# Kernel tuning notes

Hardware: AMD Instinct MI355X
Metric: run time of the kernel (lower is better)

## Reference

```python
import jax, jax.numpy as jnp
import numpy as np

MIN_C = 1e-6
MIN_NORM = 1e-15
BALL_EPS = 0.004  # float32 ball epsilon


def _norm(x):
    return jnp.maximum(jnp.linalg.norm(x, axis=-1, keepdims=True), MIN_NORM)


def _project(x, c):
    norm = _norm(x)
    maxnorm = (1.0 - BALL_EPS) / jnp.sqrt(c)
    return jnp.where(norm > maxnorm, x / norm * maxnorm, x)


def _tanh(x):
    return jnp.tanh(jnp.clip(x, -15.0, 15.0))


def _artanh(x):
    x = jnp.clip(x, -1.0 + 1e-5, 1.0 - 1e-5)
    return 0.5 * (jnp.log1p(x) - jnp.log1p(-x))


def _expmap0(u, c):
    sc = jnp.sqrt(c)
    n = _norm(u)
    return _project(_tanh(sc * n) * u / (sc * n), c)


def _logmap0(y, c):
    sc = jnp.sqrt(c)
    n = _norm(y)
    return y / n / sc * _artanh(sc * n)


def _mobius_add(x, y, c):
    x2 = jnp.sum(x * x, -1, keepdims=True)
    y2 = jnp.sum(y * y, -1, keepdims=True)
    xy = jnp.sum(x * y, -1, keepdims=True)
    num = (1 + 2 * c * xy + c * y2) * x + (1 - c * x2) * y
    den = jnp.maximum(1 + 2 * c * xy + c * c * x2 * y2, MIN_NORM)
    return num / den


N_NODE, N_EDGE, D, ATTN, B, N_VOCAB = 100000, 1000000, 64, 64, 256, 401


def setup_inputs() -> dict:
    key = jax.random.key(0)
    ks = jax.random.split(key, 12)
    r_idx = jax.random.randint(ks[0], (N_EDGE,), 0, B, dtype=jnp.int32)
    rel = jax.random.randint(ks[1], (N_EDGE,), 0, N_VOCAB, dtype=jnp.int32)
    sub = jax.random.randint(ks[2], (N_EDGE,), 0, N_NODE, dtype=jnp.int32)
    obj = jax.random.randint(ks[3], (N_EDGE,), 0, N_NODE, dtype=jnp.int32)
    zero = jnp.zeros((N_EDGE,), jnp.int32)
    edges = jnp.stack([r_idx, zero, rel, zero, sub, obj], axis=1)  # [E, 6]
    s = 0.1
    return {
        "hidden": jax.random.normal(ks[4], (N_NODE, D), jnp.float32) * s,
        "q_rel": jax.random.randint(ks[5], (B,), 0, N_VOCAB, dtype=jnp.int32),
        "edges": edges,
        "rela_embed": jax.random.normal(ks[6], (N_VOCAB, D), jnp.float32) * s,
        "Ws_w": jax.random.normal(ks[7], (ATTN, D), jnp.float32) * s,
        "Wr_w": jax.random.normal(ks[8], (ATTN, D), jnp.float32) * s,
        "Wqr_w": jax.random.normal(ks[9], (ATTN, D), jnp.float32) * s,
        "Wqr_b": jnp.zeros((ATTN,), jnp.float32),
        "Wattn_w": jax.random.normal(ks[10], (1, ATTN), jnp.float32) * s,
        "Wh_w": jax.random.normal(ks[11], (D, D), jnp.float32) * s,
        "n_node": N_NODE,
    }


def reference(hidden, q_rel, edges, rela_embed, Ws_w, Wr_w, Wqr_w, Wqr_b, Wattn_w, Wh_w, n_node):
    c = MIN_C
    sub, rel, obj, r_idx = edges[:, 4], edges[:, 2], edges[:, 5], edges[:, 0]
    hs = hidden[sub]                 # [E, D] gather
    hr = rela_embed[rel]             # [E, D]
    h_qr = rela_embed[q_rel][r_idx]  # [E, D]
    # attention MLP -> scalar gate per edge
    pre = hs @ Ws_w.T + hr @ Wr_w.T + h_qr @ Wqr_w.T + Wqr_b
    alpha = jax.nn.sigmoid(jax.nn.relu(pre) @ Wattn_w.T)  # [E, 1]
    # hyperbolic message
    hs_h = _expmap0(hs, c)
    hr_h = _expmap0(hr, c)
    mess2 = _logmap0(_project(_mobius_add(hs_h, hr_h, c), c), c)
    message = mess2 * alpha
    agg = jax.ops.segment_sum(message, obj, num_segments=n_node)  # scatter-add
    a = _expmap0(agg @ Wh_w.T, c)
    a = jax.nn.relu(a)  # act
    return _logmap0(a, c)
```

## Files before the change

kernel.cpp:

```cpp
#include <hip/hip_runtime.h>
#include <math.h>
#include <stdint.h>

#define N_NODE 100000
#define N_EDGE 1000000
#define DIM    64
#define NB     256
#define NVOCAB 401
#define SCAN_B 1024
#define NCHUNK ((N_NODE + SCAN_B - 1) / SCAN_B)
#define AGG_WAVES 8192
#define NSHARD 8
#define EPB 2048

typedef short short8  __attribute__((ext_vector_type(8)));
typedef float floatx4 __attribute__((ext_vector_type(4)));
typedef unsigned short ushort_t;

__device__ inline unsigned short f2bf_rne(float f)
{
    unsigned u = __float_as_uint(f);
    unsigned r = u + 0x7FFF + ((u >> 16) & 1);
    return (unsigned short)(r >> 16);
}
__device__ inline float bflo(unsigned u) { return __uint_as_float(u << 16); }
__device__ inline float bfhi(unsigned u) { return __uint_as_float(u & 0xFFFF0000u); }
__device__ inline unsigned short f2h(float f)
{
    _Float16 h = (_Float16)f;
    unsigned short s; __builtin_memcpy(&s, &h, 2); return s;
}
__device__ inline float h2f(unsigned b)
{
    unsigned short s = (unsigned short)b;
    _Float16 h; __builtin_memcpy(&h, &s, 2); return (float)h;
}

__device__ inline void split8(float4 v0, float4 v1, short8& hi, short8& lo)
{
    float f[8] = {v0.x, v0.y, v0.z, v0.w, v1.x, v1.y, v1.z, v1.w};
    #pragma unroll
    for (int j = 0; j < 8; ++j) {
        unsigned u = __float_as_uint(f[j]);
        unsigned r = u + 0x7FFF + ((u >> 16) & 1);
        unsigned short h = (unsigned short)(r >> 16);
        float hf = __uint_as_float(((unsigned)h) << 16);
        float l  = f[j] - hf;
        unsigned u2 = __float_as_uint(l);
        unsigned r2 = u2 + 0x7FFF + ((u2 >> 16) & 1);
        hi[j] = (short)h;
        lo[j] = (short)(r2 >> 16);
    }
}

__device__ void gemm64_body(
    const float* __restrict__ X,
    const int*   __restrict__ idx,
    const float* __restrict__ W,
    const float* __restrict__ bias,
    void* __restrict__ Yv,
    ushort_t* __restrict__ Y2,
    int R, int out_mode, int blk)
{
    int wave = threadIdx.x >> 6;
    int lane = threadIdx.x & 63;
    int m    = lane & 15;
    int quad = lane >> 4;
    int r0   = blk * 64 + wave * 16;

    int r = r0 + m;
    int src = (r < R) ? (idx ? idx[r] : r) : 0;
    const float* xrow = X + (size_t)src * DIM + quad * 8;

    float4 a0[2], a1[2];
    #pragma unroll
    for (int c = 0; c < 2; ++c) {
        a0[c] = *(const float4*)(xrow + 32 * c);
        a1[c] = *(const float4*)(xrow + 32 * c + 4);
    }
    short8 ah[2], al[2];
    #pragma unroll
    for (int c = 0; c < 2; ++c) split8(a0[c], a1[c], ah[c], al[c]);

    if (out_mode == 3 && r < R) {
        #pragma unroll
        for (int c = 0; c < 2; ++c)
            *(short8*)(Y2 + (size_t)r * DIM + 32 * c + quad * 8) = ah[c];
    }

    floatx4 acc[4] = {{0,0,0,0},{0,0,0,0},{0,0,0,0},{0,0,0,0}};
    #pragma unroll
    for (int g = 0; g < 4; ++g) {
        const float* wrow = W + (size_t)(g * 16 + m) * DIM + quad * 8;
        #pragma unroll
        for (int c = 0; c < 2; ++c) {
            float4 b0 = *(const float4*)(wrow + 32 * c);
            float4 b1 = *(const float4*)(wrow + 32 * c + 4);
            short8 bh, bl;
            split8(b0, b1, bh, bl);
            acc[g] = __builtin_amdgcn_mfma_f32_16x16x32_bf16(ah[c], bh, acc[g], 0, 0, 0);
            acc[g] = __builtin_amdgcn_mfma_f32_16x16x32_bf16(ah[c], bl, acc[g], 0, 0, 0);
            acc[g] = __builtin_amdgcn_mfma_f32_16x16x32_bf16(al[c], bh, acc[g], 0, 0, 0);
        }
    }

    #pragma unroll
    for (int g = 0; g < 4; ++g) {
        float bv = bias ? bias[g * 16 + m] : 0.0f;
        #pragma unroll
        for (int reg = 0; reg < 4; ++reg) {
            int rr = r0 + quad * 4 + reg;
            if (rr < R) {
                float v = acc[g][reg] + bv;
                if (out_mode == 1) v = fmaxf(v, 0.0f);
                if (out_mode >= 2)
                    ((ushort_t*)Yv)[(size_t)rr * DIM + g * 16 + m] = f2bf_rne(v);
                else
                    ((float*)Yv)[(size_t)rr * DIM + g * 16 + m] = v;
            }
        }
    }
}

__global__ __launch_bounds__(256) void gemm64_kernel(
    const float* __restrict__ X, const int* __restrict__ idx,
    const float* __restrict__ W, const float* __restrict__ bias,
    void* __restrict__ Yv, ushort_t* __restrict__ Y2, int R, int out_mode)
{
    gemm64_body(X, idx, W, bias, Yv, Y2, R, out_mode, blockIdx.x);
}

__global__ __launch_bounds__(256) void gemm64_bf16A_kernel(
    const ushort_t* __restrict__ A,
    const float* __restrict__ W,
    float* __restrict__ Y, int R)
{
    int wave = threadIdx.x >> 6;
    int lane = threadIdx.x & 63;
    int m    = lane & 15;
    int quad = lane >> 4;
    int r0   = blockIdx.x * 64 + wave * 16;

    int r = r0 + m;
    int src = (r < R) ? r : 0;
    short8 a8[2];
    #pragma unroll
    for (int c = 0; c < 2; ++c)
        a8[c] = *(const short8*)(A + (size_t)src * DIM + 32 * c + quad * 8);

    floatx4 acc[4] = {{0,0,0,0},{0,0,0,0},{0,0,0,0},{0,0,0,0}};
    #pragma unroll
    for (int g = 0; g < 4; ++g) {
        const float* wrow = W + (size_t)(g * 16 + m) * DIM + quad * 8;
        #pragma unroll
        for (int c = 0; c < 2; ++c) {
            float4 b0 = *(const float4*)(wrow + 32 * c);
            float4 b1 = *(const float4*)(wrow + 32 * c + 4);
            short8 bh, bl;
            split8(b0, b1, bh, bl);
            acc[g] = __builtin_amdgcn_mfma_f32_16x16x32_bf16(a8[c], bh, acc[g], 0, 0, 0);
            acc[g] = __builtin_amdgcn_mfma_f32_16x16x32_bf16(a8[c], bl, acc[g], 0, 0, 0);
        }
    }

    #pragma unroll
    for (int g = 0; g < 4; ++g) {
        #pragma unroll
        for (int reg = 0; reg < 4; ++reg) {
            int rr = r0 + quad * 4 + reg;
            if (rr < R)
                Y[(size_t)rr * DIM + g * 16 + m] = fmaxf(acc[g][reg], 0.0f);
        }
    }
}

#define G1 ((N_NODE + 63) / 64)
#define G2 ((NVOCAB + 63) / 64)
#define G3 (NB / 64)
#define GSMALL (G2 + G3)
#define GD8 ((N_EDGE + EPB - 1) / EPB)
#define PREP_T (G1 + GD8)
#define PREP_GRID (GSMALL + PREP_T)

__global__ __launch_bounds__(256) void prep_kernel(
    const float* __restrict__ hidden,
    const float* __restrict__ rela,
    const int*   __restrict__ q_rel,
    const float* __restrict__ Ws,
    const float* __restrict__ Wr,
    const float* __restrict__ Wqr,
    const float* __restrict__ Wqr_b,
    ushort_t* __restrict__ hsWs,
    ushort_t* __restrict__ hidb,
    ushort_t* __restrict__ rel_preb,
    ushort_t* __restrict__ relab,
    ushort_t* __restrict__ qr_preb,
    const int* __restrict__ edges,
    int* __restrict__ deg8,
    int* __restrict__ rank,
    int2* __restrict__ epack)
{
    int b = blockIdx.x;
    if (b < G2) {
        gemm64_body(rela, nullptr, Wr, nullptr, rel_preb, relab, NVOCAB, 3, b);
    } else if (b < GSMALL) {
        gemm64_body(rela, q_rel, Wqr, Wqr_b, qr_preb, nullptr, NB, 2, b - G2);
    } else {
        int bp = b - GSMALL;
        int prior = (int)(((long)bp * GD8) / PREP_T);
        int nxt   = (int)(((long)(bp + 1) * GD8) / PREP_T);
        if (nxt > prior) {
            int base = prior * EPB + threadIdx.x;
            #pragma unroll
            for (int k = 0; k < 8; ++k) {
                int e = base + k * 256;
                if (e < N_EDGE) {
                    int2 ab = *(const int2*)(edges + (size_t)e * 6);
                    int2 cd = *(const int2*)(edges + (size_t)e * 6 + 2);
                    int2 ef = *(const int2*)(edges + (size_t)e * 6 + 4);
                    epack[e] = make_int2(ef.x | (cd.x << 17), ef.y | (ab.x << 17));
                    int s = (e >> 11) & (NSHARD - 1);
                    rank[e] = atomicAdd(&deg8[s * N_NODE + ef.y], 1);
                }
            }
        } else {
            gemm64_body(hidden, nullptr, Ws, nullptr, hsWs, hidb, N_NODE, 3, bp - prior);
        }
    }
}

__global__ __launch_bounds__(SCAN_B) void scan1_kernel(const int* __restrict__ deg8,
                                                       int* __restrict__ partial)
{
    __shared__ int s[SCAN_B];
    int g = blockIdx.x * SCAN_B + threadIdx.x;
    int tot = 0;
    if (g < N_NODE)
        #pragma unroll
        for (int k = 0; k < NSHARD; ++k) tot += deg8[k * N_NODE + g];
    s[threadIdx.x] = tot;
    __syncthreads();
    for (int off = SCAN_B / 2; off; off >>= 1) {
        if (threadIdx.x < off) s[threadIdx.x] += s[threadIdx.x + off];
        __syncthreads();
    }
    if (threadIdx.x == 0) partial[blockIdx.x] = s[0];
}

__global__ __launch_bounds__(128) void scan2_kernel(int* __restrict__ partial, int n)
{
    __shared__ int s[128];
    int t = threadIdx.x;
    int v = (t < n) ? partial[t] : 0;
    s[t] = v;
    __syncthreads();
    for (int off = 1; off < 128; off <<= 1) {
        int add = (t >= off) ? s[t - off] : 0;
        __syncthreads();
        s[t] += add;
        __syncthreads();
    }
    if (t < n) partial[t] = s[t] - v;
}

__global__ __launch_bounds__(SCAN_B) void scan3_kernel(int* __restrict__ deg8,
                                                       const int* __restrict__ partial,
                                                       int* __restrict__ offs)
{
    __shared__ int s[SCAN_B];
    int g = blockIdx.x * SCAN_B + threadIdx.x;
    int d[NSHARD];
    int tot = 0;
    if (g < N_NODE) {
        #pragma unroll
        for (int k = 0; k < NSHARD; ++k) { d[k] = deg8[k * N_NODE + g]; tot += d[k]; }
    }
    s[threadIdx.x] = tot;
    __syncthreads();
    for (int off = 1; off < SCAN_B; off <<= 1) {
        int add = ((int)threadIdx.x >= off) ? s[threadIdx.x - off] : 0;
        __syncthreads();
        s[threadIdx.x] += add;
        __syncthreads();
    }
    if (g < N_NODE) {
        int incl = partial[blockIdx.x] + s[threadIdx.x];
        offs[g + 1] = incl;
        if (g == 0) offs[0] = 0;
        int run = incl - tot;
        #pragma unroll
        for (int k = 0; k < NSHARD; ++k) { deg8[k * N_NODE + g] = run; run += d[k]; }
    }
}

__global__ __launch_bounds__(256) void alpha_scatter_kernel(
    const int2*     __restrict__ epack,
    const int*      __restrict__ rank,
    const int*      __restrict__ base8,
    const ushort_t* __restrict__ hsWs,
    const ushort_t* __restrict__ rel_preb,
    const ushort_t* __restrict__ qr_preb,
    const float*    __restrict__ wattn,
    int2*           __restrict__ csr2)
{
    int tid = blockIdx.x * 256 + threadIdx.x;
    if (tid < 4) csr2[N_EDGE + tid] = make_int2(0, 0);

    int wave = threadIdx.x >> 6;
    int lane = threadIdx.x & 63;
    int q    = lane >> 4;
    int l    = lane & 15;
    int f0   = l * 4;
    int e0   = (blockIdx.x * 4 + wave) * 16 + q * 4;

    float4 wa = *(const float4*)(wattn + f0);

    int   sub[4], rl[4], ob[4];
    float t[4];
    #pragma unroll
    for (int j = 0; j < 4; ++j) {
        int e = e0 + j;
        int2 ep = epack[e];
        sub[j] = ep.x & 0x1FFFF;
        rl[j]  = (int)((unsigned)ep.x >> 17);
        ob[j]  = ep.y & 0x1FFFF;
        int ri = (int)((unsigned)ep.y >> 17);

        uint2 uh = *(const uint2*)(hsWs     + (size_t)sub[j] * DIM + f0);
        uint2 ur = *(const uint2*)(rel_preb + (size_t)rl[j]  * DIM + f0);
        uint2 uq = *(const uint2*)(qr_preb  + (size_t)ri     * DIM + f0);

        float tt =  fmaxf(bflo(uh.x) + bflo(ur.x) + bflo(uq.x), 0.f) * wa.x;
        tt = fmaf(fmaxf(bfhi(uh.x) + bfhi(ur.x) + bfhi(uq.x), 0.f), wa.y, tt);
        tt = fmaf(fmaxf(bflo(uh.y) + bflo(ur.y) + bflo(uq.y), 0.f), wa.z, tt);
        tt = fmaf(fmaxf(bfhi(uh.y) + bfhi(ur.y) + bfhi(uq.y), 0.f), wa.w, tt);
        t[j] = tt;
    }
    #pragma unroll
    for (int j = 0; j < 4; ++j) {
        t[j] += __shfl_xor(t[j], 1);
        t[j] += __shfl_xor(t[j], 2);
        t[j] += __shfl_xor(t[j], 4);
        t[j] += __shfl_xor(t[j], 8);
    }

    if (l == 0) {
        int4 rk = *(const int4*)(rank + e0);
        int rka[4] = {rk.x, rk.y, rk.z, rk.w};
        int sh = (e0 >> 11) & (NSHARD - 1);
        #pragma unroll
        for (int j = 0; j < 4; ++j) {
            float alpha = 1.0f / (1.0f + __expf(-t[j]));
            int slot = base8[sh * N_NODE + ob[j]] + rka[j];
            csr2[slot] = make_int2(sub[j],
                (int)(((unsigned)rl[j] << 16) | f2h(alpha)));
        }
    }
}

__global__ __launch_bounds__(256) void agg_kernel(
    const int2*     __restrict__ csr2,
    const int*      __restrict__ offs,
    const ushort_t* __restrict__ hB,
    const ushort_t* __restrict__ relab,
    ushort_t* __restrict__ aggb)
{
    int lane = threadIdx.x & 63;
    int q    = lane >> 4;
    int l    = lane & 15;
    int f0   = l * 4;
    int wv = __builtin_amdgcn_readfirstlane((blockIdx.x * blockDim.x + threadIdx.x) >> 6);

    int i   = offs[wv];
    int end = offs[wv + 1];
    for (int n = wv; n < N_NODE; n += AGG_WAVES) {
        int nn = n + AGG_WAVES;
        int ni = 0, ne = 0;
        if (nn < N_NODE) { ni = offs[nn]; ne = offs[nn + 1]; }

        float4 acc = make_float4(0.f, 0.f, 0.f, 0.f);
        int2 e0 = csr2[min(i + q,     N_EDGE + 3)];
        int2 e1 = csr2[min(i + 4 + q, N_EDGE + 3)];
        while (i < end) {
            int2 f0e = csr2[min(i + 8 + q,  N_EDGE + 3)];
            int2 f1e = csr2[min(i + 12 + q, N_EDGE + 3)];
            float v0 = (i + q < end)     ? 1.0f : 0.0f;
            float v1 = (i + 4 + q < end) ? 1.0f : 0.0f;

            unsigned ey0 = (unsigned)e0.y, ey1 = (unsigned)e1.y;
            float al0 = v0 * h2f(ey0 & 0xFFFFu);
            float al1 = v1 * h2f(ey1 & 0xFFFFu);

            uint2 uh0 = *(const uint2*)(hB    + (size_t)e0.x        * DIM + f0);
            uint2 ur0 = *(const uint2*)(relab + (size_t)(ey0 >> 16) * DIM + f0);
            uint2 uh1 = *(const uint2*)(hB    + (size_t)e1.x        * DIM + f0);
            uint2 ur1 = *(const uint2*)(relab + (size_t)(ey1 >> 16) * DIM + f0);

            acc.x = fmaf(al0, bflo(uh0.x) + bflo(ur0.x), acc.x);
            acc.y = fmaf(al0, bfhi(uh0.x) + bfhi(ur0.x), acc.y);
            acc.z = fmaf(al0, bflo(uh0.y) + bflo(ur0.y), acc.z);
            acc.w = fmaf(al0, bfhi(uh0.y) + bfhi(ur0.y), acc.w);
            acc.x = fmaf(al1, bflo(uh1.x) + bflo(ur1.x), acc.x);
            acc.y = fmaf(al1, bfhi(uh1.x) + bfhi(ur1.x), acc.y);
            acc.z = fmaf(al1, bflo(uh1.y) + bflo(ur1.y), acc.z);
            acc.w = fmaf(al1, bfhi(uh1.y) + bfhi(ur1.y), acc.w);

            e0 = f0e; e1 = f1e;
            i += 8;
        }

        acc.x += __shfl_xor(acc.x, 16); acc.x += __shfl_xor(acc.x, 32);
        acc.y += __shfl_xor(acc.y, 16); acc.y += __shfl_xor(acc.y, 32);
        acc.z += __shfl_xor(acc.z, 16); acc.z += __shfl_xor(acc.z, 32);
        acc.w += __shfl_xor(acc.w, 16); acc.w += __shfl_xor(acc.w, 32);
        if (q == 0) {
            uint2 o;
            o.x = (unsigned)f2bf_rne(acc.x) | ((unsigned)f2bf_rne(acc.y) << 16);
            o.y = (unsigned)f2bf_rne(acc.z) | ((unsigned)f2bf_rne(acc.w) << 16);
            *(uint2*)(aggb + (size_t)n * DIM + f0) = o;
        }

        i = ni; end = ne;
    }
}

__global__ __launch_bounds__(256) void edge_kernel(
    const int*      __restrict__ edges,
    const ushort_t* __restrict__ hB,
    const ushort_t* __restrict__ relab,
    const ushort_t* __restrict__ hsWs,
    const ushort_t* __restrict__ rel_preb,
    const ushort_t* __restrict__ qr_preb,
    const float*    __restrict__ wattn,
    float* __restrict__ out)
{
    int e = (blockIdx.x * blockDim.x + threadIdx.x) >> 6;
    if (e >= N_EDGE) return;
    int lane = threadIdx.x & 63;
    int r_i = edges[e * 6 + 0];
    int rl  = edges[e * 6 + 2];
    int sb  = edges[e * 6 + 4];
    int ob  = edges[e * 6 + 5];
    float hs = __uint_as_float(((unsigned)hB[(size_t)sb * DIM + lane]) << 16);
    float hr = __uint_as_float(((unsigned)relab[(size_t)rl * DIM + lane]) << 16);
    float p1 = __uint_as_float(((unsigned)hsWs[(size_t)sb * DIM + lane]) << 16);
    float p2 = __uint_as_float(((unsigned)rel_preb[(size_t)rl * DIM + lane]) << 16);
    float p3 = __uint_as_float(((unsigned)qr_preb[(size_t)r_i * DIM + lane]) << 16);
    float t = wattn[lane] * fmaxf(p1 + p2 + p3, 0.0f);
    #pragma unroll
    for (int off = 32; off; off >>= 1) t += __shfl_xor(t, off);
    float alpha = 1.0f / (1.0f + __expf(-t));
    atomicAdd(&out[(size_t)ob * DIM + lane], (hs + hr) * alpha);
}

extern "C" void kernel_launch(void* const* d_in, const int* in_sizes, int n_in,
                              void* d_out, int out_size, void* d_ws, size_t ws_size,
                              hipStream_t stream)
{
    const float* hidden = (const float*)d_in[0];
    const int*   q_rel  = (const int*)  d_in[1];
    const int*   edges  = (const int*)  d_in[2];
    const float* rela   = (const float*)d_in[3];
    const float* Ws     = (const float*)d_in[4];
    const float* Wr     = (const float*)d_in[5];
    const float* Wqr    = (const float*)d_in[6];
    const float* Wqr_b  = (const float*)d_in[7];
    const float* Wattn  = (const float*)d_in[8];
    const float* Wh     = (const float*)d_in[9];
    float* out = (float*)d_out;

    ushort_t* qr_preb  = (ushort_t*)d_ws;
    ushort_t* rel_preb = qr_preb + NB * DIM;
    ushort_t* relab    = rel_preb + NVOCAB * DIM;
    ushort_t* hsWs     = relab + NVOCAB * DIM;
    ushort_t* hidb     = hsWs + (size_t)N_NODE * DIM;
    int2* epack  = (int2*)(((uintptr_t)(hidb + (size_t)N_NODE * DIM) + 15) & ~(uintptr_t)15);
    int*  rank   = (int*)(epack + N_EDGE);
    int*  deg8   = rank + N_EDGE;
    int*  offs   = deg8 + NSHARD * N_NODE;
    int*  partial= offs + (N_NODE + 1);
    int2* csr2   = (int2*)(((uintptr_t)(partial + 128) + 15) & ~(uintptr_t)15);
    size_t csr_need = ((char*)(csr2 + N_EDGE + 4)) - (char*)d_ws;
    bool use_csr = ws_size >= csr_need;
    ushort_t* aggb = (ushort_t*)epack;

    if (use_csr) {
        hipMemsetAsync(deg8, 0, NSHARD * N_NODE * sizeof(int), stream);
        prep_kernel<<<PREP_GRID, 256, 0, stream>>>(
            hidden, rela, q_rel, Ws, Wr, Wqr, Wqr_b,
            hsWs, hidb, rel_preb, relab, qr_preb, edges, deg8, rank, epack);
        scan1_kernel<<<NCHUNK, SCAN_B, 0, stream>>>(deg8, partial);
        scan2_kernel<<<1, 128, 0, stream>>>(partial, NCHUNK);
        scan3_kernel<<<NCHUNK, SCAN_B, 0, stream>>>(deg8, partial, offs);
        alpha_scatter_kernel<<<N_EDGE / 64, 256, 0, stream>>>(
            epack, rank, deg8, hsWs, rel_preb, qr_preb, Wattn, csr2);
        agg_kernel<<<AGG_WAVES / 4, 256, 0, stream>>>(csr2, offs, hidb, relab, aggb);
        gemm64_bf16A_kernel<<<(N_NODE + 63) / 64, 256, 0, stream>>>(aggb, Wh, out, N_NODE);
    } else {
        gemm64_kernel<<<(NVOCAB + 63) / 64, 256, 0, stream>>>(
            rela, nullptr, Wr, nullptr, rel_preb, relab, NVOCAB, 3);
        gemm64_kernel<<<(NB + 63) / 64, 256, 0, stream>>>(
            rela, q_rel, Wqr, Wqr_b, qr_preb, nullptr, NB, 2);
        gemm64_kernel<<<(N_NODE + 63) / 64, 256, 0, stream>>>(
            hidden, nullptr, Ws, nullptr, hsWs, hidb, N_NODE, 3);
        hipMemsetAsync(d_out, 0, (size_t)N_NODE * DIM * sizeof(float), stream);
        edge_kernel<<<(N_EDGE + 3) / 4, 256, 0, stream>>>(
            edges, hidb, relab, hsWs, rel_preb, qr_preb, Wattn, out);
        gemm64_kernel<<<(N_NODE + 63) / 64, 256, 0, stream>>>(
            out, nullptr, Wh, nullptr, out, nullptr, N_NODE, 1);
    }
}
```

Measured before the change: 258.3 us.

## Pre-split weights to bf16 hi/lo once and vectorize GEMM output stores

Adds an init kernel that zeroes the degree counters (replacing the memset) and converts Ws, Wr, Wqr and Wh into bf16 hi/lo pairs once, so the GEMM blocks stop redoing that conversion per wave. The GEMMs swap MFMA operand order so each lane holds four consecutive output columns, which allows float4 and uint2 stores instead of scattered scalar stores. The alpha scatter is spread across four lanes instead of one lane looping. The change needs slightly more workspace, and if the workspace is too small the slower fallback path is used.

```diff
diff --git a/kernel.cpp b/kernel.cpp
--- a/kernel.cpp
+++ b/kernel.cpp
@@ -53,6 +53,151 @@
     }
 }
 
+#define INIT_GRID ((NSHARD * N_NODE + 255) / 256)
+
+__global__ __launch_bounds__(256) void init_kernel(
+    const float* __restrict__ Ws, const float* __restrict__ Wr,
+    const float* __restrict__ Wqr, const float* __restrict__ Wh,
+    ushort_t* __restrict__ wsp, int* __restrict__ deg8)
+{
+    int tid = blockIdx.x * 256 + threadIdx.x;
+    if (tid < NSHARD * N_NODE) deg8[tid] = 0;
+    if (tid < 4 * 4096) {
+        int w = tid >> 12, e = tid & 4095;
+        const float* src = (w == 0) ? Ws : (w == 1) ? Wr : (w == 2) ? Wqr : Wh;
+        float f = src[e];
+        unsigned u = __float_as_uint(f);
+        unsigned r = u + 0x7FFF + ((u >> 16) & 1);
+        unsigned short h = (unsigned short)(r >> 16);
+        float hf = __uint_as_float(((unsigned)h) << 16);
+        float l  = f - hf;
+        unsigned u2 = __float_as_uint(l);
+        unsigned r2 = u2 + 0x7FFF + ((u2 >> 16) & 1);
+        wsp[w * 8192 + e]        = h;
+        wsp[w * 8192 + 4096 + e] = (unsigned short)(r2 >> 16);
+    }
+}
+
+__device__ void gemm64p_body(
+    const float* __restrict__ X,
+    const int*   __restrict__ idx,
+    const ushort_t* __restrict__ Whi,
+    const ushort_t* __restrict__ Wlo,
+    const float* __restrict__ bias,
+    void* __restrict__ Yv,
+    ushort_t* __restrict__ Y2,
+    int R, int out_mode, int blk)
+{
+    int wave = threadIdx.x >> 6;
+    int lane = threadIdx.x & 63;
+    int m    = lane & 15;
+    int quad = lane >> 4;
+    int r0   = blk * 64 + wave * 16;
+
+    int r = r0 + m;
+    int src = (r < R) ? (idx ? idx[r] : r) : 0;
+    const float* xrow = X + (size_t)src * DIM + quad * 8;
+
+    float4 a0[2], a1[2];
+    #pragma unroll
+    for (int c = 0; c < 2; ++c) {
+        a0[c] = *(const float4*)(xrow + 32 * c);
+        a1[c] = *(const float4*)(xrow + 32 * c + 4);
+    }
+    short8 ah[2], al[2];
+    #pragma unroll
+    for (int c = 0; c < 2; ++c) split8(a0[c], a1[c], ah[c], al[c]);
+
+    if (out_mode == 3 && r < R) {
+        #pragma unroll
+        for (int c = 0; c < 2; ++c)
+            *(short8*)(Y2 + (size_t)r * DIM + 32 * c + quad * 8) = ah[c];
+    }
+
+    floatx4 acc[4] = {{0,0,0,0},{0,0,0,0},{0,0,0,0},{0,0,0,0}};
+    #pragma unroll
+    for (int g = 0; g < 4; ++g) {
+        const ushort_t* whrow = Whi + (size_t)(g * 16 + m) * DIM + quad * 8;
+        const ushort_t* wlrow = Wlo + (size_t)(g * 16 + m) * DIM + quad * 8;
+        #pragma unroll
+        for (int c = 0; c < 2; ++c) {
+            short8 bh = *(const short8*)(whrow + 32 * c);
+            short8 bl = *(const short8*)(wlrow + 32 * c);
+            acc[g] = __builtin_amdgcn_mfma_f32_16x16x32_bf16(bh, ah[c], acc[g], 0, 0, 0);
+            acc[g] = __builtin_amdgcn_mfma_f32_16x16x32_bf16(bl, ah[c], acc[g], 0, 0, 0);
+            acc[g] = __builtin_amdgcn_mfma_f32_16x16x32_bf16(bh, al[c], acc[g], 0, 0, 0);
+        }
+    }
+
+    if (r < R) {
+        #pragma unroll
+        for (int g = 0; g < 4; ++g) {
+            float4 bv = make_float4(0.f, 0.f, 0.f, 0.f);
+            if (bias) bv = *(const float4*)(bias + g * 16 + quad * 4);
+            float v0 = acc[g][0] + bv.x;
+            float v1 = acc[g][1] + bv.y;
+            float v2 = acc[g][2] + bv.z;
+            float v3 = acc[g][3] + bv.w;
+            if (out_mode == 1) {
+                v0 = fmaxf(v0, 0.f); v1 = fmaxf(v1, 0.f);
+                v2 = fmaxf(v2, 0.f); v3 = fmaxf(v3, 0.f);
+            }
+            if (out_mode >= 2) {
+                uint2 o;
+                o.x = (unsigned)f2bf_rne(v0) | ((unsigned)f2bf_rne(v1) << 16);
+                o.y = (unsigned)f2bf_rne(v2) | ((unsigned)f2bf_rne(v3) << 16);
+                *(uint2*)((ushort_t*)Yv + (size_t)r * DIM + g * 16 + quad * 4) = o;
+            } else {
+                *(float4*)((float*)Yv + (size_t)r * DIM + g * 16 + quad * 4) =
+                    make_float4(v0, v1, v2, v3);
+            }
+        }
+    }
+}
+
+__global__ __launch_bounds__(256) void gemm64p_bf16A_kernel(
+    const ushort_t* __restrict__ A,
+    const ushort_t* __restrict__ Whi,
+    const ushort_t* __restrict__ Wlo,
+    float* __restrict__ Y, int R)
+{
+    int wave = threadIdx.x >> 6;
+    int lane = threadIdx.x & 63;
+    int m    = lane & 15;
+    int quad = lane >> 4;
+    int r0   = blockIdx.x * 64 + wave * 16;
+
+    int r = r0 + m;
+    int src = (r < R) ? r : 0;
+    short8 a8[2];
+    #pragma unroll
+    for (int c = 0; c < 2; ++c)
+        a8[c] = *(const short8*)(A + (size_t)src * DIM + 32 * c + quad * 8);
+
+    floatx4 acc[4] = {{0,0,0,0},{0,0,0,0},{0,0,0,0},{0,0,0,0}};
+    #pragma unroll
+    for (int g = 0; g < 4; ++g) {
+        const ushort_t* whrow = Whi + (size_t)(g * 16 + m) * DIM + quad * 8;
+        const ushort_t* wlrow = Wlo + (size_t)(g * 16 + m) * DIM + quad * 8;
+        #pragma unroll
+        for (int c = 0; c < 2; ++c) {
+            short8 bh = *(const short8*)(whrow + 32 * c);
+            short8 bl = *(const short8*)(wlrow + 32 * c);
+            acc[g] = __builtin_amdgcn_mfma_f32_16x16x32_bf16(bh, a8[c], acc[g], 0, 0, 0);
+            acc[g] = __builtin_amdgcn_mfma_f32_16x16x32_bf16(bl, a8[c], acc[g], 0, 0, 0);
+        }
+    }
+
+    if (r < R) {
+        #pragma unroll
+        for (int g = 0; g < 4; ++g) {
+            *(float4*)(Y + (size_t)r * DIM + g * 16 + quad * 4) =
+                make_float4(fmaxf(acc[g][0], 0.f), fmaxf(acc[g][1], 0.f),
+                            fmaxf(acc[g][2], 0.f), fmaxf(acc[g][3], 0.f));
+        }
+    }
+}
+
 __device__ void gemm64_body(
     const float* __restrict__ X,
     const int*   __restrict__ idx,
@@ -130,50 +275,6 @@
     gemm64_body(X, idx, W, bias, Yv, Y2, R, out_mode, blockIdx.x);
 }
 
-__global__ __launch_bounds__(256) void gemm64_bf16A_kernel(
-    const ushort_t* __restrict__ A,
-    const float* __restrict__ W,
-    float* __restrict__ Y, int R)
-{
-    int wave = threadIdx.x >> 6;
-    int lane = threadIdx.x & 63;
-    int m    = lane & 15;
-    int quad = lane >> 4;
-    int r0   = blockIdx.x * 64 + wave * 16;
-
-    int r = r0 + m;
-    int src = (r < R) ? r : 0;
-    short8 a8[2];
-    #pragma unroll
-    for (int c = 0; c < 2; ++c)
-        a8[c] = *(const short8*)(A + (size_t)src * DIM + 32 * c + quad * 8);
-
-    floatx4 acc[4] = {{0,0,0,0},{0,0,0,0},{0,0,0,0},{0,0,0,0}};
-    #pragma unroll
-    for (int g = 0; g < 4; ++g) {
-        const float* wrow = W + (size_t)(g * 16 + m) * DIM + quad * 8;
-        #pragma unroll
-        for (int c = 0; c < 2; ++c) {
-            float4 b0 = *(const float4*)(wrow + 32 * c);
-            float4 b1 = *(const float4*)(wrow + 32 * c + 4);
-            short8 bh, bl;
-            split8(b0, b1, bh, bl);
-            acc[g] = __builtin_amdgcn_mfma_f32_16x16x32_bf16(a8[c], bh, acc[g], 0, 0, 0);
-            acc[g] = __builtin_amdgcn_mfma_f32_16x16x32_bf16(a8[c], bl, acc[g], 0, 0, 0);
-        }
-    }
-
-    #pragma unroll
-    for (int g = 0; g < 4; ++g) {
-        #pragma unroll
-        for (int reg = 0; reg < 4; ++reg) {
-            int rr = r0 + quad * 4 + reg;
-            if (rr < R)
-                Y[(size_t)rr * DIM + g * 16 + m] = fmaxf(acc[g][reg], 0.0f);
-        }
-    }
-}
-
 #define G1 ((N_NODE + 63) / 64)
 #define G2 ((NVOCAB + 63) / 64)
 #define G3 (NB / 64)
@@ -186,9 +287,7 @@
     const float* __restrict__ hidden,
     const float* __restrict__ rela,
     const int*   __restrict__ q_rel,
-    const float* __restrict__ Ws,
-    const float* __restrict__ Wr,
-    const float* __restrict__ Wqr,
+    const ushort_t* __restrict__ wsp,
     const float* __restrict__ Wqr_b,
     ushort_t* __restrict__ hsWs,
     ushort_t* __restrict__ hidb,
@@ -202,9 +301,11 @@
 {
     int b = blockIdx.x;
     if (b < G2) {
-        gemm64_body(rela, nullptr, Wr, nullptr, rel_preb, relab, NVOCAB, 3, b);
+        gemm64p_body(rela, nullptr, wsp + 1 * 8192, wsp + 1 * 8192 + 4096,
+                     nullptr, rel_preb, relab, NVOCAB, 3, b);
     } else if (b < GSMALL) {
-        gemm64_body(rela, q_rel, Wqr, Wqr_b, qr_preb, nullptr, NB, 2, b - G2);
+        gemm64p_body(rela, q_rel, wsp + 2 * 8192, wsp + 2 * 8192 + 4096,
+                     Wqr_b, qr_preb, nullptr, NB, 2, b - G2);
     } else {
         int bp = b - GSMALL;
         int prior = (int)(((long)bp * GD8) / PREP_T);
@@ -224,7 +325,8 @@
                 }
             }
         } else {
-            gemm64_body(hidden, nullptr, Ws, nullptr, hsWs, hidb, N_NODE, 3, bp - prior);
+            gemm64p_body(hidden, nullptr, wsp, wsp + 4096,
+                         nullptr, hsWs, hidb, N_NODE, 3, bp - prior);
         }
     }
 }
@@ -344,17 +446,13 @@
         t[j] += __shfl_xor(t[j], 8);
     }
 
-    if (l == 0) {
-        int4 rk = *(const int4*)(rank + e0);
-        int rka[4] = {rk.x, rk.y, rk.z, rk.w};
+    if (l < 4) {
+        int j = l;
         int sh = (e0 >> 11) & (NSHARD - 1);
-        #pragma unroll
-        for (int j = 0; j < 4; ++j) {
-            float alpha = 1.0f / (1.0f + __expf(-t[j]));
-            int slot = base8[sh * N_NODE + ob[j]] + rka[j];
-            csr2[slot] = make_int2(sub[j],
-                (int)(((unsigned)rl[j] << 16) | f2h(alpha)));
-        }
+        float alpha = 1.0f / (1.0f + __expf(-t[j]));
+        int slot = base8[sh * N_NODE + ob[j]] + rank[e0 + j];
+        csr2[slot] = make_int2(sub[j],
+            (int)(((unsigned)rl[j] << 16) | f2h(alpha)));
     }
 }
 
@@ -480,14 +578,15 @@
     int*  offs   = deg8 + NSHARD * N_NODE;
     int*  partial= offs + (N_NODE + 1);
     int2* csr2   = (int2*)(((uintptr_t)(partial + 128) + 15) & ~(uintptr_t)15);
-    size_t csr_need = ((char*)(csr2 + N_EDGE + 4)) - (char*)d_ws;
+    ushort_t* wsp = (ushort_t*)(csr2 + N_EDGE + 4);
+    size_t csr_need = ((char*)(wsp + 4 * 8192)) - (char*)d_ws;
     bool use_csr = ws_size >= csr_need;
     ushort_t* aggb = (ushort_t*)epack;
 
     if (use_csr) {
-        hipMemsetAsync(deg8, 0, NSHARD * N_NODE * sizeof(int), stream);
+        init_kernel<<<INIT_GRID, 256, 0, stream>>>(Ws, Wr, Wqr, Wh, wsp, deg8);
         prep_kernel<<<PREP_GRID, 256, 0, stream>>>(
-            hidden, rela, q_rel, Ws, Wr, Wqr, Wqr_b,
+            hidden, rela, q_rel, wsp, Wqr_b,
             hsWs, hidb, rel_preb, relab, qr_preb, edges, deg8, rank, epack);
         scan1_kernel<<<NCHUNK, SCAN_B, 0, stream>>>(deg8, partial);
         scan2_kernel<<<1, 128, 0, stream>>>(partial, NCHUNK);
@@ -495,7 +594,8 @@
         alpha_scatter_kernel<<<N_EDGE / 64, 256, 0, stream>>>(
             epack, rank, deg8, hsWs, rel_preb, qr_preb, Wattn, csr2);
         agg_kernel<<<AGG_WAVES / 4, 256, 0, stream>>>(csr2, offs, hidb, relab, aggb);
-        gemm64_bf16A_kernel<<<(N_NODE + 63) / 64, 256, 0, stream>>>(aggb, Wh, out, N_NODE);
+        gemm64p_bf16A_kernel<<<(N_NODE + 63) / 64, 256, 0, stream>>>(
+            aggb, wsp + 3 * 8192, wsp + 3 * 8192 + 4096, out, N_NODE);
     } else {
         gemm64_kernel<<<(NVOCAB + 63) / 64, 256, 0, stream>>>(
             rela, nullptr, Wr, nullptr, rel_preb, relab, NVOCAB, 3);
```

Result: no change. 262.6 us (+1.7%).
